# Kernel optimization log

Measured on AMD Instinct MI355X. Metric: run time of the kernel, lower is better.

Reference implementation:

```python
import jax, jax.numpy as jnp
import numpy as np

NUM_LAYERS = 4
D_MODEL = 2
N_HALF = 32  # d_state // 2 complex modes
B, L = 512, 10000


def setup_inputs() -> dict:
    key = jax.random.key(0)
    ks = jax.random.split(key, 10)
    x = jax.random.normal(ks[0], (B, L, 3), dtype=jnp.float32)
    W1 = jax.random.normal(ks[1], (2, 3), dtype=jnp.float32) / np.float32(np.sqrt(3.0))
    b1 = jax.random.normal(ks[2], (2,), dtype=jnp.float32) * 0.1
    W2 = jax.random.normal(ks[3], (2, 2), dtype=jnp.float32) / np.float32(np.sqrt(2.0))
    b2 = jax.random.normal(ks[4], (2,), dtype=jnp.float32) * 0.1
    # S4D kernel params (stacked over layers)
    dt_min, dt_max = 1e-3, 1e-1
    log_dt = (jax.random.uniform(ks[5], (NUM_LAYERS, D_MODEL), dtype=jnp.float32)
              * np.float32(np.log(dt_max) - np.log(dt_min)) + np.float32(np.log(dt_min)))
    log_A_real = jnp.log(0.5 * jnp.ones((NUM_LAYERS, D_MODEL, N_HALF), dtype=jnp.float32))
    A_imag = (np.float32(np.pi) * jnp.arange(N_HALF, dtype=jnp.float32)
              * jnp.ones((NUM_LAYERS, D_MODEL, 1), dtype=jnp.float32))
    C = jax.random.normal(ks[6], (NUM_LAYERS, D_MODEL, N_HALF, 2), dtype=jnp.float32) * np.float32(0.5 ** 0.5)
    D = jax.random.normal(ks[7], (NUM_LAYERS, D_MODEL), dtype=jnp.float32)
    Wout = jax.random.normal(ks[8], (NUM_LAYERS, 2 * D_MODEL, D_MODEL), dtype=jnp.float32) / np.float32(np.sqrt(D_MODEL))
    bout = jax.random.normal(ks[9], (NUM_LAYERS, 2 * D_MODEL), dtype=jnp.float32) * 0.1
    return dict(x=x, W1=W1, b1=b1, W2=W2, b2=b2, log_dt=log_dt,
                log_A_real=log_A_real, A_imag=A_imag, C=C, D=D, Wout=Wout, bout=bout)


def _s4d_kernel(log_dt, log_A_real, A_imag, C, Lk):
    # log_dt: (H,), log_A_real/A_imag: (H,N), C: (H,N,2) -> kernel (H,Lk)
    dt = jnp.exp(log_dt)                              # (H,)
    Cc = C[..., 0] + 1j * C[..., 1]                   # (H,N) complex
    A = -jnp.exp(log_A_real) + 1j * A_imag            # (H,N)
    dtA = A * dt[:, None]                             # (H,N)
    K = dtA[:, :, None] * jnp.arange(Lk)              # (H,N,Lk)
    Cn = Cc * (jnp.exp(dtA) - 1.0) / A                # (H,N)
    return 2.0 * jnp.einsum('hn,hnl->hl', Cn, jnp.exp(K)).real


def reference(x, W1, b1, W2, b2, log_dt, log_A_real, A_imag, C, D, Wout, bout):
    Lseq = x.shape[1]
    h = x @ W1.T + b1                                 # (B,L,2)
    u = jnp.transpose(h, (0, 2, 1))                   # (B,H,L)
    for i in range(NUM_LAYERS):
        k = _s4d_kernel(log_dt[i], log_A_real[i], A_imag[i], C[i], Lseq)  # (H,L)
        kf = jnp.fft.rfft(k, n=2 * Lseq)              # (H,L+1)
        uf = jnp.fft.rfft(u, n=2 * Lseq)              # (B,H,L+1)
        y = jnp.fft.irfft(uf * kf, n=2 * Lseq)[..., :Lseq]  # linear conv via 2L FFT
        y = y + u * D[i][:, None]                     # skip connection
        y = jax.nn.gelu(y, approximate=False)
        y = jnp.einsum('oh,bhl->bol', Wout[i], y) + bout[i][None, :, None]  # Conv1d(H,2H,1)
        a, g = jnp.split(y, 2, axis=1)                # GLU over channel dim
        u = a * jax.nn.sigmoid(g)
    h = jnp.transpose(u, (0, 2, 1))                   # (B,L,2)
    return h @ W2.T + b2
```

## Files before the change

kernel.cpp:

```cpp
#include <hip/hip_runtime.h>
#include <hip/hip_bf16.h>
#include <math.h>

#define BB 512
#define LL 10000
#define HH 2
#define NN 32
#define NL 4
#define TT 64
#define CHK 157
#define CPAD 160
#define BL (BB*LL)

#define OFF_U0   0
#define OFF_U1   10240000
#define OFF_S0   20480000
#define OFF_S1   30769152
#define OFF_TAB  41058304

typedef _Float16 half8 __attribute__((ext_vector_type(8)));
typedef float f32x4 __attribute__((ext_vector_type(4)));

__global__ void setup_kernel(const float* __restrict__ log_dt,
                             const float* __restrict__ log_A_real,
                             const float* __restrict__ A_imag,
                             const float* __restrict__ Cin,
                             float* __restrict__ lam, float* __restrict__ lamT,
                             float* __restrict__ Cn, float* __restrict__ Kt,
                             float* __restrict__ P) {
    int ih = blockIdx.x;
    int tid = threadIdx.x;
    __shared__ float s_dtA[NN * 2];
    __shared__ float s_Cn[NN * 2];
    float dt = expf(log_dt[ih]);
    if (tid < NN) {
        int n = tid;
        float aRe = -expf(log_A_real[ih * NN + n]);
        float aIm = A_imag[ih * NN + n];
        float dRe = aRe * dt, dIm = aIm * dt;
        s_dtA[2 * n] = dRe; s_dtA[2 * n + 1] = dIm;
        float e = expf(dRe);
        float sn, cs; sincosf(dIm, &sn, &cs);
        float lRe = e * cs, lIm = e * sn;
        lam[ih * NN * 2 + 2 * n] = lRe;
        lam[ih * NN * 2 + 2 * n + 1] = lIm;
        float eT = expf((float)TT * dRe);
        float snT, csT; sincosf((float)TT * dIm, &snT, &csT);
        lamT[ih * NN * 2 + 2 * n] = eT * csT;
        lamT[ih * NN * 2 + 2 * n + 1] = eT * snT;
        float C0 = Cin[(ih * NN + n) * 2];
        float C1 = Cin[(ih * NN + n) * 2 + 1];
        float numRe = lRe - 1.0f, numIm = lIm;
        float den = aRe * aRe + aIm * aIm;
        float qRe = (numRe * aRe + numIm * aIm) / den;
        float qIm = (numIm * aRe - numRe * aIm) / den;
        float cnRe = C0 * qRe - C1 * qIm;
        float cnIm = C0 * qIm + C1 * qRe;
        Cn[ih * NN * 2 + 2 * n] = cnRe;
        Cn[ih * NN * 2 + 2 * n + 1] = cnIm;
        s_Cn[2 * n] = cnRe; s_Cn[2 * n + 1] = cnIm;
        for (int l = 0; l < TT; l++) {
            float p = (float)(l + 1);
            float ee = expf(p * dRe);
            float ss, cc; sincosf(p * dIm, &ss, &cc);
            P[(ih * NN + n) * TT * 2 + 2 * l]     = ee * cc;
            P[(ih * NN + n) * TT * 2 + 2 * l + 1] = ee * ss;
        }
    }
    __syncthreads();
    int d = tid;
    float acc = 0.0f;
    for (int n = 0; n < NN; n++) {
        float dRe = s_dtA[2 * n], dIm = s_dtA[2 * n + 1];
        float ee = expf((float)d * dRe);
        float ss, cc; sincosf((float)d * dIm, &ss, &cc);
        acc += s_Cn[2 * n] * (ee * cc) - s_Cn[2 * n + 1] * (ee * ss);
    }
    Kt[ih * TT + d] = 2.0f * acc;
}

__global__ void setup2_kernel(const float* __restrict__ Kt,
                              const float* __restrict__ P,
                              _Float16* __restrict__ AF,
                              _Float16* __restrict__ EF) {
    int ih = blockIdx.x;
    int lane = threadIdx.x;
    for (int kt = 0; kt < 4; kt++) {
        for (int lt = 0; lt < 4; lt++) {
            int l = lt * 16 + (lane & 15);
            int kbase = kt * 32 + (lane >> 4) * 8;
            for (int j = 0; j < 8; j++) {
                int k = kbase + j;
                float v;
                if (k < 64) {
                    int d = l - k;
                    v = (d >= 0) ? Kt[ih * TT + d] : 0.0f;
                } else {
                    int j2 = k - 64;
                    int n = j2 >> 1;
                    float pre = P[(ih * NN + n) * TT * 2 + 2 * l];
                    float pim = P[(ih * NN + n) * TT * 2 + 2 * l + 1];
                    v = (j2 & 1) ? (-2.0f * pim) : (2.0f * pre);
                }
                float hi = __uint_as_float(__float_as_uint(v) & 0xFFFFE000u);
                float lo = v - hi;
                size_t o0 = ((((size_t)ih * 2 + 0) * 4 + kt) * 4 + lt) * 512 + lane * 8 + j;
                size_t o1 = ((((size_t)ih * 2 + 1) * 4 + kt) * 4 + lt) * 512 + lane * 8 + j;
                AF[o0] = (_Float16)hi;
                AF[o1] = (_Float16)lo;
            }
        }
    }
    for (int kt = 0; kt < 2; kt++) {
        for (int lt = 0; lt < 4; lt++) {
            int row = lt * 16 + (lane & 15);
            int n = row >> 1, isIm = row & 1;
            int kbase = kt * 32 + (lane >> 4) * 8;
            for (int j = 0; j < 8; j++) {
                int k = kbase + j;
                int pw = 63 - k;
                float v;
                if (pw == 0) v = isIm ? 0.0f : 1.0f;
                else v = P[(ih * NN + n) * TT * 2 + 2 * (pw - 1) + isIm];
                float hi = __uint_as_float(__float_as_uint(v) & 0xFFFFE000u);
                float lo = v - hi;
                size_t o0 = ((((size_t)ih * 2 + 0) * 2 + kt) * 4 + lt) * 512 + lane * 8 + j;
                size_t o1 = ((((size_t)ih * 2 + 1) * 2 + kt) * 4 + lt) * 512 + lane * 8 + j;
                EF[o0] = (_Float16)hi;
                EF[o1] = (_Float16)lo;
            }
        }
    }
}

__global__ __launch_bounds__(256) void embed_kernel(const float* __restrict__ x,
                             const float* __restrict__ W1, const float* __restrict__ b1,
                             float* __restrict__ u) {
    int idx = blockIdx.x * blockDim.x + threadIdx.x;
    if (idx >= BL) return;
    int b = idx / LL, l = idx - b * LL;
    float x0 = x[idx * 3], x1 = x[idx * 3 + 1], x2 = x[idx * 3 + 2];
    float u0 = fmaf(W1[0], x0, fmaf(W1[1], x1, fmaf(W1[2], x2, b1[0])));
    float u1 = fmaf(W1[3], x0, fmaf(W1[4], x1, fmaf(W1[5], x2, b1[1])));
    u[(b * HH + 0) * LL + l] = u0;
    u[(b * HH + 1) * LL + l] = u1;
}

__device__ __forceinline__ void splitB(const f32x4& f0, const f32x4& f1,
                                       half8& Bh, half8& Bl) {
#pragma unroll
    for (int e = 0; e < 8; e++) {
        float v = (e < 4) ? f0[e] : f1[e - 4];
        float hi = __uint_as_float(__float_as_uint(v) & 0xFFFFE000u);
        Bh[e] = (_Float16)hi;
        Bl[e] = (_Float16)(v - hi);
    }
}

__global__ __launch_bounds__(256) void phaseA_mfma(const float* __restrict__ u,
                              const _Float16* __restrict__ EF,
                              float* __restrict__ stRaw) {
    const int wv = threadIdx.x >> 6;
    const int lane = threadIdx.x & 63;
    const int quad = lane >> 4;
    const int li = lane & 15;
    const int gw = blockIdx.x * 4 + wv;
    const int col = gw * 16 + li;
    const int b = col / CPAD;
    const int c = col - b * CPAD;
    const int cc = (c < CHK) ? c : (CHK - 1);
    const float* uB = u + (size_t)(b * HH) * LL + cc * TT;

    f32x4 eacc[4][2];
#pragma unroll
    for (int lt = 0; lt < 4; lt++)
#pragma unroll
        for (int ch = 0; ch < 2; ch++) eacc[lt][ch] = (f32x4){0.f, 0.f, 0.f, 0.f};

#pragma unroll
    for (int ch = 0; ch < 2; ch++) {
#pragma unroll
        for (int kt = 0; kt < 2; kt++) {
            const float* src = uB + ch * LL + kt * 32 + quad * 8;
            f32x4 f0 = *(const f32x4*)src;
            f32x4 f1 = *(const f32x4*)(src + 4);
            half8 Bh, Bl; splitB(f0, f1, Bh, Bl);
            const _Float16* efb = EF + (size_t)ch * 8192 + kt * 2048 + lane * 8;
#pragma unroll
            for (int lt = 0; lt < 4; lt++) {
                half8 Eh = *(const half8*)(efb + lt * 512);
                half8 El = *(const half8*)(efb + 4096 + lt * 512);
                eacc[lt][ch] = __builtin_amdgcn_mfma_f32_16x16x32_f16(Eh, Bh, eacc[lt][ch], 0, 0, 0);
                eacc[lt][ch] = __builtin_amdgcn_mfma_f32_16x16x32_f16(Eh, Bl, eacc[lt][ch], 0, 0, 0);
                eacc[lt][ch] = __builtin_amdgcn_mfma_f32_16x16x32_f16(El, Bh, eacc[lt][ch], 0, 0, 0);
            }
        }
    }
    if (c < CHK) {
        float* sp = stRaw + ((size_t)b * CHK + c) * 128;
#pragma unroll
        for (int ch = 0; ch < 2; ch++)
#pragma unroll
            for (int lt = 0; lt < 4; lt++)
                *(f32x4*)(sp + ch * 64 + lt * 16 + quad * 4) = eacc[lt][ch];
    }
}

__global__ __launch_bounds__(64) void phaseB_kernel(const float* __restrict__ lamT,
                              const float* __restrict__ CnT,
                              const float* __restrict__ stRaw,
                              float* __restrict__ stW, int layer) {
    int b = blockIdx.x;
    int lane = threadIdx.x;
    int h = lane >> 5, n = lane & 31;
    float lRe = lamT[(layer * HH + h) * NN * 2 + 2 * n];
    float lIm = lamT[(layer * HH + h) * NN * 2 + 2 * n + 1];
    float cRe = CnT[(layer * HH + h) * NN * 2 + 2 * n];
    float cIm = CnT[(layer * HH + h) * NN * 2 + 2 * n + 1];
    const float2* src = (const float2*)(stRaw + (size_t)b * CHK * 128) + lane;
    float2* dst = (float2*)(stW + (size_t)b * CHK * 128) + lane;
    float2 buf[8];
#pragma unroll
    for (int p = 0; p < 8; p++) buf[p] = src[(size_t)p * 64];
    float rRe = 0.f, rIm = 0.f;
    for (int co = 0; co < 20; co++) {
#pragma unroll
        for (int ci = 0; ci < 8; ci++) {
            int cx = co * 8 + ci;
            if (cx < CHK) {
                float2 v = buf[ci];
                if (cx + 8 < CHK) buf[ci] = src[(size_t)(cx + 8) * 64];
                float2 w;
                w.x = cRe * rRe - cIm * rIm;
                w.y = cRe * rIm + cIm * rRe;
                dst[(size_t)cx * 64] = w;
                float tRe = fmaf(lRe, rRe, fmaf(-lIm, rIm, v.x));
                float tIm = fmaf(lRe, rIm, fmaf(lIm, rRe, v.y));
                rRe = tRe; rIm = tIm;
            }
        }
    }
}

__global__ __launch_bounds__(256) void phaseC_mfma(
        const float* __restrict__ u, float* __restrict__ uNext,
        const _Float16* __restrict__ AF, const _Float16* __restrict__ EF,
        const float* __restrict__ stW, float* __restrict__ stRaw,
        const float* __restrict__ Dp, const float* __restrict__ Wout,
        const float* __restrict__ bout, int layer,
        const float* __restrict__ W2, const float* __restrict__ b2,
        float* __restrict__ out, int isLast) {
    const int wv = threadIdx.x >> 6;
    const int lane = threadIdx.x & 63;
    const int quad = lane >> 4;
    const int li = lane & 15;
    const int gw = blockIdx.x * 4 + wv;
    const int col = gw * 16 + li;
    const int b = col / CPAD;
    const int c = col - b * CPAD;
    const int cc = (c < CHK) ? c : (CHK - 1);
    const float* uB = u + (size_t)(b * HH) * LL + cc * TT;
    const float* wB = stW + ((size_t)b * CHK + cc) * 128;

    f32x4 acc[4][2];
#pragma unroll
    for (int lt = 0; lt < 4; lt++)
#pragma unroll
        for (int ch = 0; ch < 2; ch++) acc[lt][ch] = (f32x4){0.f, 0.f, 0.f, 0.f};

#pragma unroll
    for (int kt = 0; kt < 4; kt++) {
#pragma unroll
        for (int ch = 0; ch < 2; ch++) {
            const _Float16* afb = AF + (size_t)(layer * 2 + ch) * 16384 + kt * 2048 + lane * 8;
            const float* src = (kt < 2)
                ? (uB + ch * LL + kt * 32 + quad * 8)
                : (wB + ch * 64 + (kt - 2) * 32 + quad * 8);
            f32x4 f0 = *(const f32x4*)src;
            f32x4 f1 = *(const f32x4*)(src + 4);
            half8 Bh, Bl; splitB(f0, f1, Bh, Bl);
#pragma unroll
            for (int lt = 0; lt < 4; lt++) {
                half8 Ah = *(const half8*)(afb + lt * 512);
                half8 Al = *(const half8*)(afb + 8192 + lt * 512);
                acc[lt][ch] = __builtin_amdgcn_mfma_f32_16x16x32_f16(Ah, Bh, acc[lt][ch], 0, 0, 0);
                acc[lt][ch] = __builtin_amdgcn_mfma_f32_16x16x32_f16(Ah, Bl, acc[lt][ch], 0, 0, 0);
                acc[lt][ch] = __builtin_amdgcn_mfma_f32_16x16x32_f16(Al, Bh, acc[lt][ch], 0, 0, 0);
            }
        }
    }

    float D0 = Dp[layer * HH + 0], D1 = Dp[layer * HH + 1];
    const float* Wo = Wout + layer * 8;
    const float* bo = bout + layer * 4;
    bool cOK = (c < CHK);
    f32x4 r0f[4], r1f[4];
#pragma unroll
    for (int lt = 0; lt < 4; lt++) {
        int l = lt * 16 + quad * 4;
        f32x4 u0 = *(const f32x4*)(uB + l);
        f32x4 u1 = *(const f32x4*)(uB + LL + l);
        f32x4 r0, r1;
#pragma unroll
        for (int r = 0; r < 4; r++) {
            float a0 = fmaf(D0, u0[r], acc[lt][0][r]);
            float a1 = fmaf(D1, u1[r], acc[lt][1][r]);
            a0 = 0.5f * a0 * (1.0f + erff(a0 * 0.70710678118654752f));
            a1 = 0.5f * a1 * (1.0f + erff(a1 * 0.70710678118654752f));
            float z0 = fmaf(Wo[0], a0, fmaf(Wo[1], a1, bo[0]));
            float z1 = fmaf(Wo[2], a0, fmaf(Wo[3], a1, bo[1]));
            float z2 = fmaf(Wo[4], a0, fmaf(Wo[5], a1, bo[2]));
            float z3 = fmaf(Wo[6], a0, fmaf(Wo[7], a1, bo[3]));
            float g2 = 1.0f / (1.0f + expf(-z2));
            float g3 = 1.0f / (1.0f + expf(-z3));
            r0[r] = z0 * g2;
            r1[r] = z1 * g3;
        }
        r0f[lt] = r0; r1f[lt] = r1;
        bool ok = cOK && (c < CHK - 1 || lt == 0);
        if (!isLast) {
            if (ok) {
                float* p0 = uNext + (size_t)(b * HH) * LL + cc * TT + l;
                *(f32x4*)p0 = r0;
                *(f32x4*)(p0 + LL) = r1;
            }
        } else {
            if (ok) {
                float w20 = W2[0], w21 = W2[1], w22 = W2[2], w23 = W2[3];
                float b20 = b2[0], b21 = b2[1];
                float* op = out + ((size_t)b * LL + (size_t)cc * TT + l) * 2;
                f32x4 lo4, hi4;
                lo4[0] = fmaf(r0[0], w20, fmaf(r1[0], w21, b20));
                lo4[1] = fmaf(r0[0], w22, fmaf(r1[0], w23, b21));
                lo4[2] = fmaf(r0[1], w20, fmaf(r1[1], w21, b20));
                lo4[3] = fmaf(r0[1], w22, fmaf(r1[1], w23, b21));
                hi4[0] = fmaf(r0[2], w20, fmaf(r1[2], w21, b20));
                hi4[1] = fmaf(r0[2], w22, fmaf(r1[2], w23, b21));
                hi4[2] = fmaf(r0[3], w20, fmaf(r1[3], w21, b20));
                hi4[3] = fmaf(r0[3], w22, fmaf(r1[3], w23, b21));
                *(f32x4*)op = lo4;
                *(f32x4*)(op + 4) = hi4;
            }
        }
    }

    if (!isLast) {
        f32x4 rmA[4], rmB[4];
#pragma unroll
        for (int lt = 0; lt < 4; lt++) {
            bool z = (c == CHK - 1) && (lt > 0);
            rmA[lt] = z ? (f32x4){0.f, 0.f, 0.f, 0.f} : r0f[lt];
            rmB[lt] = z ? (f32x4){0.f, 0.f, 0.f, 0.f} : r1f[lt];
        }
        f32x4 eacc[4][2];
#pragma unroll
        for (int lt = 0; lt < 4; lt++)
#pragma unroll
            for (int ch = 0; ch < 2; ch++) eacc[lt][ch] = (f32x4){0.f, 0.f, 0.f, 0.f};

#pragma unroll
        for (int ch = 0; ch < 2; ch++) {
#pragma unroll
            for (int kt = 0; kt < 2; kt++) {
                float bv[8];
#pragma unroll
                for (int j = 0; j < 8; j++) {
                    int srcLane = ((quad & 1) * 2 + (j >> 2)) * 16 + li;
                    float x0 = ch ? rmB[kt * 2 + 0][j & 3] : rmA[kt * 2 + 0][j & 3];
                    float x1 = ch ? rmB[kt * 2 + 1][j & 3] : rmA[kt * 2 + 1][j & 3];
                    float a = __shfl(x0, srcLane, 64);
                    float bb = __shfl(x1, srcLane, 64);
                    bv[j] = (quad & 2) ? bb : a;
                }
                half8 Bh, Bl;
#pragma unroll
                for (int e = 0; e < 8; e++) {
                    float v = bv[e];
                    float hi = __uint_as_float(__float_as_uint(v) & 0xFFFFE000u);
                    Bh[e] = (_Float16)hi;
                    Bl[e] = (_Float16)(v - hi);
                }
                const _Float16* efb = EF + (size_t)layer * 16384 + (layer >= 0 ? 0 : 0)
                                      + (size_t)(ch + 1 - 1) * 0;
                efb = EF + ((size_t)(layer + 1) * 2 + ch) * 8192 + kt * 2048 + lane * 8;
#pragma unroll
                for (int lt = 0; lt < 4; lt++) {
                    half8 Eh = *(const half8*)(efb + lt * 512);
                    half8 El = *(const half8*)(efb + 4096 + lt * 512);
                    eacc[lt][ch] = __builtin_amdgcn_mfma_f32_16x16x32_f16(Eh, Bh, eacc[lt][ch], 0, 0, 0);
                    eacc[lt][ch] = __builtin_amdgcn_mfma_f32_16x16x32_f16(Eh, Bl, eacc[lt][ch], 0, 0, 0);
                    eacc[lt][ch] = __builtin_amdgcn_mfma_f32_16x16x32_f16(El, Bh, eacc[lt][ch], 0, 0, 0);
                }
            }
        }
        if (cOK) {
            float* sp = stRaw + ((size_t)b * CHK + c) * 128;
#pragma unroll
            for (int ch = 0; ch < 2; ch++)
#pragma unroll
                for (int lt = 0; lt < 4; lt++)
                    *(f32x4*)(sp + ch * 64 + lt * 16 + quad * 4) = eacc[lt][ch];
        }
    }
}

extern "C" void kernel_launch(void* const* d_in, const int* in_sizes, int n_in,
                              void* d_out, int out_size, void* d_ws, size_t ws_size,
                              hipStream_t stream) {
    const float* x         = (const float*)d_in[0];
    const float* W1        = (const float*)d_in[1];
    const float* b1        = (const float*)d_in[2];
    const float* W2        = (const float*)d_in[3];
    const float* b2        = (const float*)d_in[4];
    const float* log_dt    = (const float*)d_in[5];
    const float* log_A_real= (const float*)d_in[6];
    const float* A_imag    = (const float*)d_in[7];
    const float* Cin       = (const float*)d_in[8];
    const float* Dp        = (const float*)d_in[9];
    const float* Wout      = (const float*)d_in[10];
    const float* bout      = (const float*)d_in[11];
    float* out = (float*)d_out;
    float* ws = (float*)d_ws;

    float* U0   = ws + OFF_U0;
    float* U1   = ws + OFF_U1;
    float* S0   = ws + OFF_S0;
    float* S1   = ws + OFF_S1;
    float* lam  = ws + OFF_TAB;
    float* lamT = lam + 512;
    float* Cn   = lamT + 512;
    float* Kt   = Cn + 512;
    float* P    = Kt + 512;
    _Float16* AF = (_Float16*)(P + 32768);
    _Float16* EF = AF + 131072;

    setup_kernel<<<dim3(NL * HH), dim3(64), 0, stream>>>(log_dt, log_A_real, A_imag, Cin,
                                                         lam, lamT, Cn, Kt, P);
    setup2_kernel<<<dim3(NL * HH), dim3(64), 0, stream>>>(Kt, P, AF, EF);
    embed_kernel<<<dim3(BL / 256), dim3(256), 0, stream>>>(x, W1, b1, U0);
    phaseA_mfma<<<dim3(BB * CPAD / 64), dim3(256), 0, stream>>>(U0, EF, S0);

    float* cur = U0;
    float* nxt = U1;
    for (int i = 0; i < NL; i++) {
        phaseB_kernel<<<dim3(BB), dim3(64), 0, stream>>>(lamT, Cn, S0, S1, i);
        phaseC_mfma<<<dim3(BB * CPAD / 64), dim3(256), 0, stream>>>(cur, nxt, AF, EF, S1, S0,
                                                                    Dp, Wout, bout, i,
                                                                    W2, b2, out,
                                                                    (i == NL - 1) ? 1 : 0);
        float* tmp = cur; cur = nxt; nxt = tmp;
    }
}
```

Before: 438.8 us.

## Vectorize embed, pre-split state to fp16 in phaseB, shrink blocks to one wave

The embed kernel now processes four positions per thread with float4 loads and vector stores. phaseB writes the weighted state as pre-split fp16 hi/lo pairs, so phaseC loads half8 directly instead of re-splitting fp32. It also uses a deeper 16-entry prefetch buffer. phaseA and phaseC switch from 4-wave to single-wave blocks, and phaseC hoists all B-operand loads ahead of the MFMA loop. These changes cut memory traffic and ALU work per tile, at the cost of more blocks and higher register use.

```diff
diff --git a/kernel.cpp b/kernel.cpp
--- a/kernel.cpp
+++ b/kernel.cpp
@@ -19,6 +19,7 @@
 #define OFF_TAB  41058304
 
 typedef _Float16 half8 __attribute__((ext_vector_type(8)));
+typedef _Float16 half2v __attribute__((ext_vector_type(2)));
 typedef float f32x4 __attribute__((ext_vector_type(4)));
 
 __global__ void setup_kernel(const float* __restrict__ log_dt,
@@ -137,13 +138,28 @@
                              const float* __restrict__ W1, const float* __restrict__ b1,
                              float* __restrict__ u) {
     int idx = blockIdx.x * blockDim.x + threadIdx.x;
-    if (idx >= BL) return;
-    int b = idx / LL, l = idx - b * LL;
-    float x0 = x[idx * 3], x1 = x[idx * 3 + 1], x2 = x[idx * 3 + 2];
-    float u0 = fmaf(W1[0], x0, fmaf(W1[1], x1, fmaf(W1[2], x2, b1[0])));
-    float u1 = fmaf(W1[3], x0, fmaf(W1[4], x1, fmaf(W1[5], x2, b1[1])));
-    u[(b * HH + 0) * LL + l] = u0;
-    u[(b * HH + 1) * LL + l] = u1;
+    int b = idx / (LL / 4), l4 = idx - b * (LL / 4);
+    int l = l4 * 4;
+    const float4* xp = (const float4*)(x + ((size_t)b * LL + l) * 3);
+    float4 xa = xp[0], xb = xp[1], xc = xp[2];
+    float w10 = W1[0], w11 = W1[1], w12 = W1[2];
+    float w13 = W1[3], w14 = W1[4], w15 = W1[5];
+    float bb0 = b1[0], bb1 = b1[1];
+    float t0[3] = {xa.x, xa.y, xa.z};
+    float t1[3] = {xa.w, xb.x, xb.y};
+    float t2[3] = {xb.z, xb.w, xc.x};
+    float t3[3] = {xc.y, xc.z, xc.w};
+    f32x4 u0, u1;
+    u0[0] = fmaf(w10, t0[0], fmaf(w11, t0[1], fmaf(w12, t0[2], bb0)));
+    u0[1] = fmaf(w10, t1[0], fmaf(w11, t1[1], fmaf(w12, t1[2], bb0)));
+    u0[2] = fmaf(w10, t2[0], fmaf(w11, t2[1], fmaf(w12, t2[2], bb0)));
+    u0[3] = fmaf(w10, t3[0], fmaf(w11, t3[1], fmaf(w12, t3[2], bb0)));
+    u1[0] = fmaf(w13, t0[0], fmaf(w14, t0[1], fmaf(w15, t0[2], bb1)));
+    u1[1] = fmaf(w13, t1[0], fmaf(w14, t1[1], fmaf(w15, t1[2], bb1)));
+    u1[2] = fmaf(w13, t2[0], fmaf(w14, t2[1], fmaf(w15, t2[2], bb1)));
+    u1[3] = fmaf(w13, t3[0], fmaf(w14, t3[1], fmaf(w15, t3[2], bb1)));
+    *(f32x4*)(u + (size_t)(b * HH) * LL + l) = u0;
+    *(f32x4*)(u + (size_t)(b * HH + 1) * LL + l) = u1;
 }
 
 __device__ __forceinline__ void splitB(const f32x4& f0, const f32x4& f1,
@@ -157,15 +173,13 @@
     }
 }
 
-__global__ __launch_bounds__(256) void phaseA_mfma(const float* __restrict__ u,
+__global__ __launch_bounds__(64) void phaseA_mfma(const float* __restrict__ u,
                               const _Float16* __restrict__ EF,
                               float* __restrict__ stRaw) {
-    const int wv = threadIdx.x >> 6;
-    const int lane = threadIdx.x & 63;
+    const int lane = threadIdx.x;
     const int quad = lane >> 4;
     const int li = lane & 15;
-    const int gw = blockIdx.x * 4 + wv;
-    const int col = gw * 16 + li;
+    const int col = blockIdx.x * 16 + li;
     const int b = col / CPAD;
     const int c = col - b * CPAD;
     const int cc = (c < CHK) ? c : (CHK - 1);
@@ -209,7 +223,7 @@
 __global__ __launch_bounds__(64) void phaseB_kernel(const float* __restrict__ lamT,
                               const float* __restrict__ CnT,
                               const float* __restrict__ stRaw,
-                              float* __restrict__ stW, int layer) {
+                              _Float16* __restrict__ stW, int layer) {
     int b = blockIdx.x;
     int lane = threadIdx.x;
     int h = lane >> 5, n = lane & 31;
@@ -218,22 +232,26 @@
     float cRe = CnT[(layer * HH + h) * NN * 2 + 2 * n];
     float cIm = CnT[(layer * HH + h) * NN * 2 + 2 * n + 1];
     const float2* src = (const float2*)(stRaw + (size_t)b * CHK * 128) + lane;
-    float2* dst = (float2*)(stW + (size_t)b * CHK * 128) + lane;
-    float2 buf[8];
-#pragma unroll
-    for (int p = 0; p < 8; p++) buf[p] = src[(size_t)p * 64];
+    _Float16* dst = stW + (size_t)b * CHK * 256 + 2 * lane;
+    float2 buf[16];
+#pragma unroll
+    for (int p = 0; p < 16; p++) buf[p] = src[(size_t)p * 64];
     float rRe = 0.f, rIm = 0.f;
-    for (int co = 0; co < 20; co++) {
-#pragma unroll
-        for (int ci = 0; ci < 8; ci++) {
-            int cx = co * 8 + ci;
+    for (int co = 0; co < 10; co++) {
+#pragma unroll
+        for (int ci = 0; ci < 16; ci++) {
+            int cx = co * 16 + ci;
             if (cx < CHK) {
                 float2 v = buf[ci];
-                if (cx + 8 < CHK) buf[ci] = src[(size_t)(cx + 8) * 64];
-                float2 w;
-                w.x = cRe * rRe - cIm * rIm;
-                w.y = cRe * rIm + cIm * rRe;
-                dst[(size_t)cx * 64] = w;
+                if (cx + 16 < CHK) buf[ci] = src[(size_t)(cx + 16) * 64];
+                float wRe = cRe * rRe - cIm * rIm;
+                float wIm = cRe * rIm + cIm * rRe;
+                float hRe = __uint_as_float(__float_as_uint(wRe) & 0xFFFFE000u);
+                float hIm = __uint_as_float(__float_as_uint(wIm) & 0xFFFFE000u);
+                half2v hv = {(_Float16)hRe, (_Float16)hIm};
+                half2v lv = {(_Float16)(wRe - hRe), (_Float16)(wIm - hIm)};
+                *(half2v*)(dst + (size_t)cx * 256) = hv;
+                *(half2v*)(dst + (size_t)cx * 256 + 128) = lv;
                 float tRe = fmaf(lRe, rRe, fmaf(-lIm, rIm, v.x));
                 float tIm = fmaf(lRe, rIm, fmaf(lIm, rRe, v.y));
                 rRe = tRe; rIm = tIm;
@@ -242,25 +260,49 @@
     }
 }
 
-__global__ __launch_bounds__(256) void phaseC_mfma(
+__global__ __launch_bounds__(64) void phaseC_mfma(
         const float* __restrict__ u, float* __restrict__ uNext,
         const _Float16* __restrict__ AF, const _Float16* __restrict__ EF,
-        const float* __restrict__ stW, float* __restrict__ stRaw,
+        const _Float16* __restrict__ stW, float* __restrict__ stRaw,
         const float* __restrict__ Dp, const float* __restrict__ Wout,
         const float* __restrict__ bout, int layer,
         const float* __restrict__ W2, const float* __restrict__ b2,
         float* __restrict__ out, int isLast) {
-    const int wv = threadIdx.x >> 6;
-    const int lane = threadIdx.x & 63;
+    const int lane = threadIdx.x;
     const int quad = lane >> 4;
     const int li = lane & 15;
-    const int gw = blockIdx.x * 4 + wv;
-    const int col = gw * 16 + li;
+    const int col = blockIdx.x * 16 + li;
     const int b = col / CPAD;
     const int c = col - b * CPAD;
     const int cc = (c < CHK) ? c : (CHK - 1);
     const float* uB = u + (size_t)(b * HH) * LL + cc * TT;
-    const float* wB = stW + ((size_t)b * CHK + cc) * 128;
+    const _Float16* wB = stW + ((size_t)b * CHK + cc) * 256;
+
+    f32x4 uf[2][2][2];
+#pragma unroll
+    for (int ch = 0; ch < 2; ch++)
+#pragma unroll
+        for (int kt = 0; kt < 2; kt++) {
+            const float* s = uB + ch * LL + kt * 32 + quad * 8;
+            uf[ch][kt][0] = *(const f32x4*)s;
+            uf[ch][kt][1] = *(const f32x4*)(s + 4);
+        }
+    half8 wbh[2][2], wbl[2][2];
+#pragma unroll
+    for (int ch = 0; ch < 2; ch++)
+#pragma unroll
+        for (int k2 = 0; k2 < 2; k2++) {
+            const _Float16* s = wB + ch * 64 + k2 * 32 + quad * 8;
+            wbh[ch][k2] = *(const half8*)s;
+            wbl[ch][k2] = *(const half8*)(s + 128);
+        }
+
+    half8 uh[2][2], ul[2][2];
+#pragma unroll
+    for (int ch = 0; ch < 2; ch++)
+#pragma unroll
+        for (int kt = 0; kt < 2; kt++)
+            splitB(uf[ch][kt][0], uf[ch][kt][1], uh[ch][kt], ul[ch][kt]);
 
     f32x4 acc[4][2];
 #pragma unroll
@@ -273,12 +315,8 @@
 #pragma unroll
         for (int ch = 0; ch < 2; ch++) {
             const _Float16* afb = AF + (size_t)(layer * 2 + ch) * 16384 + kt * 2048 + lane * 8;
-            const float* src = (kt < 2)
-                ? (uB + ch * LL + kt * 32 + quad * 8)
-                : (wB + ch * 64 + (kt - 2) * 32 + quad * 8);
-            f32x4 f0 = *(const f32x4*)src;
-            f32x4 f1 = *(const f32x4*)(src + 4);
-            half8 Bh, Bl; splitB(f0, f1, Bh, Bl);
+            half8 Bh = (kt < 2) ? uh[ch][kt] : wbh[ch][kt - 2];
+            half8 Bl = (kt < 2) ? ul[ch][kt] : wbl[ch][kt - 2];
 #pragma unroll
             for (int lt = 0; lt < 4; lt++) {
                 half8 Ah = *(const half8*)(afb + lt * 512);
@@ -380,9 +418,8 @@
                     Bh[e] = (_Float16)hi;
                     Bl[e] = (_Float16)(v - hi);
                 }
-                const _Float16* efb = EF + (size_t)layer * 16384 + (layer >= 0 ? 0 : 0)
-                                      + (size_t)(ch + 1 - 1) * 0;
-                efb = EF + ((size_t)(layer + 1) * 2 + ch) * 8192 + kt * 2048 + lane * 8;
+                const _Float16* efb = EF + ((size_t)(layer + 1) * 2 + ch) * 8192
+                                      + kt * 2048 + lane * 8;
 #pragma unroll
                 for (int lt = 0; lt < 4; lt++) {
                     half8 Eh = *(const half8*)(efb + lt * 512);
@@ -425,7 +462,7 @@
     float* U0   = ws + OFF_U0;
     float* U1   = ws + OFF_U1;
     float* S0   = ws + OFF_S0;
-    float* S1   = ws + OFF_S1;
+    _Float16* S1 = (_Float16*)(ws + OFF_S1);
     float* lam  = ws + OFF_TAB;
     float* lamT = lam + 512;
     float* Cn   = lamT + 512;
@@ -437,17 +474,17 @@
     setup_kernel<<<dim3(NL * HH), dim3(64), 0, stream>>>(log_dt, log_A_real, A_imag, Cin,
                                                          lam, lamT, Cn, Kt, P);
     setup2_kernel<<<dim3(NL * HH), dim3(64), 0, stream>>>(Kt, P, AF, EF);
-    embed_kernel<<<dim3(BL / 256), dim3(256), 0, stream>>>(x, W1, b1, U0);
-    phaseA_mfma<<<dim3(BB * CPAD / 64), dim3(256), 0, stream>>>(U0, EF, S0);
+    embed_kernel<<<dim3(BL / 4 / 256), dim3(256), 0, stream>>>(x, W1, b1, U0);
+    phaseA_mfma<<<dim3(BB * CPAD / 16), dim3(64), 0, stream>>>(U0, EF, S0);
 
     float* cur = U0;
     float* nxt = U1;
     for (int i = 0; i < NL; i++) {
         phaseB_kernel<<<dim3(BB), dim3(64), 0, stream>>>(lamT, Cn, S0, S1, i);
-        phaseC_mfma<<<dim3(BB * CPAD / 64), dim3(256), 0, stream>>>(cur, nxt, AF, EF, S1, S0,
-                                                                    Dp, Wout, bout, i,
-                                                                    W2, b2, out,
-                                                                    (i == NL - 1) ? 1 : 0);
+        phaseC_mfma<<<dim3(BB * CPAD / 16), dim3(64), 0, stream>>>(cur, nxt, AF, EF, S1, S0,
+                                                                   Dp, Wout, bout, i,
+                                                                   W2, b2, out,
+                                                                   (i == NL - 1) ? 1 : 0);
         float* tmp = cur; cur = nxt; nxt = tmp;
     }
 }
```

New measurement: 442.5 us. Within noise of the previous version (+0.8%).
